# Optimization experiments

Measured on AMD Instinct MI355X. Metric: run time of the kernel, lower is better.

Reference implementation:

```python
import jax, jax.numpy as jnp
import numpy as np

B, T, E, H, V = 64, 32, 512, 512, 32000


def setup_inputs() -> dict:
    key = jax.random.key(0)
    ks = jax.random.split(key, 9)
    s = 0.05
    return {
        "features": jax.random.normal(ks[0], (B, E), jnp.float32),
        "captions": jax.random.randint(ks[1], (B, T), 0, V),
        "seq_len": T,
        "embed_table": jax.random.normal(ks[2], (V, E), jnp.float32) * s,
        "W_ih": jax.random.normal(ks[3], (4 * H, E), jnp.float32) * s,
        "W_hh": jax.random.normal(ks[4], (4 * H, H), jnp.float32) * s,
        "b_ih": jax.random.normal(ks[5], (4 * H,), jnp.float32) * s,
        "b_hh": jax.random.normal(ks[6], (4 * H,), jnp.float32) * s,
        "W_out": jax.random.normal(ks[7], (V, H), jnp.float32) * s,
        "b_out": jax.random.normal(ks[8], (V,), jnp.float32) * s,
    }


def _lstm_cell(x, h, c, W_ih, W_hh, b_ih, b_hh):
    # gates: (B, 4H), PyTorch LSTMCell gate order i, f, g, o
    gates = x @ W_ih.T + b_ih + h @ W_hh.T + b_hh
    i, f, g, o = jnp.split(gates, 4, axis=-1)
    c_new = jax.nn.sigmoid(f) * c + jax.nn.sigmoid(i) * jnp.tanh(g)
    h_new = jax.nn.sigmoid(o) * jnp.tanh(c_new)
    return h_new, c_new


def reference(features, captions, seq_len, embed_table, W_ih, W_hh, b_ih, b_hh, W_out, b_out):
    batch = features.shape[0]
    hdim = W_hh.shape[1]
    h0 = jnp.zeros((batch, hdim), features.dtype)
    c0 = jnp.zeros((batch, hdim), features.dtype)
    # prime the state with image features
    h, c = _lstm_cell(features, h0, c0, W_ih, W_hh, b_ih, b_hh)

    cap_emb = embed_table[captions]          # (B, T, E)
    xs = jnp.swapaxes(cap_emb, 0, 1)         # (T, B, E) for scan

    def step(carry, x_t):
        h, c = carry
        h, c = _lstm_cell(x_t, h, c, W_ih, W_hh, b_ih, b_hh)
        # dropout is identity in eval mode
        out = h @ W_out.T + b_out             # (B, V)
        return (h, c), out

    _, outs = jax.lax.scan(step, (h, c), xs)  # (T, B, V)
    return jnp.swapaxes(outs, 0, 1)           # (B, T, V)
```

## Files before the change

kernel.cpp:

```cpp
#include <hip/hip_runtime.h>
#include <stdint.h>

#define BB 64
#define TT 32
#define EE 512
#define HH 512
#define VV 32000
#define G4 2048

typedef _Float16 f16x8 __attribute__((ext_vector_type(8)));
typedef float f32x4 __attribute__((ext_vector_type(4)));

__device__ __forceinline__ unsigned short f2h(float f) {
  return __builtin_bit_cast(unsigned short, (_Float16)f);
}
__device__ __forceinline__ void gload_lds16(const unsigned short* g, unsigned short* l) {
  __builtin_amdgcn_global_load_lds((const __attribute__((address_space(1))) void*)g,
                                   (__attribute__((address_space(3))) void*)l, 16, 0, 0);
}
__device__ __forceinline__ float sigm(float x) { return 1.f / (1.f + __expf(-x)); }
__device__ __forceinline__ float tanh_fast(float x) {
  return 1.f - 2.f / (__expf(2.f * x) + 1.f);
}

__global__ __launch_bounds__(256) void k_gemm_ih(const float* __restrict__ feat,
                                                 const int* __restrict__ cap,
                                                 const float* __restrict__ emb,
                                                 const float* __restrict__ Bw,
                                                 const float* __restrict__ bih,
                                                 const float* __restrict__ bhh,
                                                 float* __restrict__ C) {
  __shared__ float As[16][128];
  __shared__ float Bs[16][128];
  const int tid = threadIdx.x;
  const int bx = blockIdx.x & 15;
  const int by = blockIdx.x >> 4;
  const int m0 = by * 128, n0 = bx * 128;
  const int tx = tid & 15, ty = tid >> 4;

  float acc[8][8];
#pragma unroll
  for (int i = 0; i < 8; i++)
#pragma unroll
    for (int j = 0; j < 8; j++) acc[i][j] = 0.f;

  const int lr = tid >> 1;
  const int lk = (tid & 1) * 8;
  int arow = m0 + lr; if (arow > 2111) arow = 2111;
  const float* Ap;
  if (arow < BB) {
    Ap = feat + (size_t)arow * EE + lk;
  } else {
    int idx = arow - BB;
    int t = idx >> 6, b = idx & 63;
    Ap = emb + (size_t)cap[b * TT + t] * EE + lk;
  }
  const int brow = n0 + lr;
  const float* Bp = Bw + (size_t)brow * EE + lk;

  for (int k0 = 0; k0 < EE; k0 += 16) {
    float4 a0 = *(const float4*)(Ap + k0);
    float4 a1 = *(const float4*)(Ap + k0 + 4);
    float4 b0 = *(const float4*)(Bp + k0);
    float4 b1 = *(const float4*)(Bp + k0 + 4);
    __syncthreads();
    As[lk + 0][lr] = a0.x; As[lk + 1][lr] = a0.y; As[lk + 2][lr] = a0.z; As[lk + 3][lr] = a0.w;
    As[lk + 4][lr] = a1.x; As[lk + 5][lr] = a1.y; As[lk + 6][lr] = a1.z; As[lk + 7][lr] = a1.w;
    Bs[lk + 0][lr] = b0.x; Bs[lk + 1][lr] = b0.y; Bs[lk + 2][lr] = b0.z; Bs[lk + 3][lr] = b0.w;
    Bs[lk + 4][lr] = b1.x; Bs[lk + 5][lr] = b1.y; Bs[lk + 6][lr] = b1.z; Bs[lk + 7][lr] = b1.w;
    __syncthreads();
#pragma unroll
    for (int k = 0; k < 16; k++) {
      float a[8], b[8];
      *(float4*)&a[0] = *(const float4*)&As[k][ty * 8];
      *(float4*)&a[4] = *(const float4*)&As[k][ty * 8 + 4];
      *(float4*)&b[0] = *(const float4*)&Bs[k][tx * 8];
      *(float4*)&b[4] = *(const float4*)&Bs[k][tx * 8 + 4];
#pragma unroll
      for (int i = 0; i < 8; i++)
#pragma unroll
        for (int j = 0; j < 8; j++) acc[i][j] += a[i] * b[j];
    }
  }

  float bs[8];
#pragma unroll
  for (int j = 0; j < 8; j++) {
    int n = n0 + tx * 8 + j;
    bs[j] = bih[n] + bhh[n];
  }
#pragma unroll
  for (int i = 0; i < 8; i++) {
    int m = m0 + ty * 8 + i;
    if (m < 2112) {
      float4 o0, o1;
      o0.x = acc[i][0] + bs[0]; o0.y = acc[i][1] + bs[1];
      o0.z = acc[i][2] + bs[2]; o0.w = acc[i][3] + bs[3];
      o1.x = acc[i][4] + bs[4]; o1.y = acc[i][5] + bs[5];
      o1.z = acc[i][6] + bs[6]; o1.w = acc[i][7] + bs[7];
      *(float4*)(C + (size_t)m * G4 + n0 + tx * 8) = o0;
      *(float4*)(C + (size_t)m * G4 + n0 + tx * 8 + 4) = o1;
    }
  }
}

__global__ void k_zero(int* ctr) {
  if (threadIdx.x < 33)
    __hip_atomic_store(&ctr[threadIdx.x], 0, __ATOMIC_RELAXED, __HIP_MEMORY_SCOPE_AGENT);
}

__global__ __launch_bounds__(512) void k_fused(const float* __restrict__ Gpre,
                                               const float* __restrict__ Whh,
                                               const float* __restrict__ Wout,
                                               const float* __restrict__ bout,
                                               char* hseq_base,
                                               float* __restrict__ out,
                                               int* __restrict__ ctr) {
  __shared__ __align__(16) char lds_raw[65536];
  unsigned short* hseq16 = (unsigned short*)hseq_base;
  unsigned int* hseq32 = (unsigned int*)hseq_base;

  const int tid = threadIdx.x;
  const int bid = blockIdx.x;
  const int l = tid & 63;
  const int w = tid >> 6;

  if (bid < 64) {
    unsigned short* W_lds = (unsigned short*)lds_raw;
    float* gate_buf = (float*)(lds_raw + 32768);
    const int u0 = bid * 8;
    const int lr = l & 15;
    const int kc = l >> 4;
    const int nt = w & 1;
    const int mt = w >> 1;
    const int es = w * 8 + (l >> 3);
    const int edu = l & 7;

    {
      int row = tid >> 4;
      int sub = tid & 15;
      int g = row >> 3, du = row & 7;
      const float* srcp = Whh + (size_t)(g * 512 + u0 + du) * HH;
#pragma unroll
      for (int c0 = 0; c0 < 4; ++c0) {
        int c = sub * 4 + c0;
        float4 va = *(const float4*)(srcp + c * 8);
        float4 vb = *(const float4*)(srcp + c * 8 + 4);
        __align__(16) unsigned short t8[8];
        t8[0] = f2h(va.x); t8[1] = f2h(va.y); t8[2] = f2h(va.z); t8[3] = f2h(va.w);
        t8[4] = f2h(vb.x); t8[5] = f2h(vb.y); t8[6] = f2h(vb.z); t8[7] = f2h(vb.w);
        *(int4*)((char*)W_lds + row * 1024 + ((c ^ (row & 7)) * 16)) = *(const int4*)t8;
      }
    }

    float c_reg;
    {
      const float* gp = Gpre + (size_t)es * G4 + u0 + edu;
      float gi = gp[0], gg = gp[1024], go = gp[1536];
      float cn = sigm(gi) * tanh_fast(gg);
      float hn = sigm(go) * tanh_fast(cn);
      c_reg = cn;
      unsigned int hb = f2h(hn);
      unsigned int other = (unsigned int)__shfl_xor((int)hb, 1);
      if (!(l & 1))
        __hip_atomic_store(&hseq32[(size_t)es * 256 + bid * 4 + (edu >> 1)],
                           hb | (other << 16), __ATOMIC_RELAXED, __HIP_MEMORY_SCOPE_AGENT);
    }
    asm volatile("s_waitcnt vmcnt(0)" ::: "memory");
    __syncthreads();
    if (tid == 0)
      __hip_atomic_fetch_add(&ctr[0], 1, __ATOMIC_RELAXED, __HIP_MEMORY_SCOPE_AGENT);

    float pre[4];
#pragma unroll
    for (int g = 0; g < 4; ++g)
      pre[g] = Gpre[((size_t)64 + es) * G4 + g * 512 + u0 + edu];

    if (tid == 0) {
      while (__hip_atomic_load(&ctr[0], __ATOMIC_RELAXED, __HIP_MEMORY_SCOPE_AGENT) < 64)
        __builtin_amdgcn_s_sleep(1);
    }
    __syncthreads();

    for (int s = 1; s <= TT; ++s) {
      const unsigned short* hin = hseq16 + (size_t)(s - 1) * BB * HH;
      f32x4 acca = {0.f, 0.f, 0.f, 0.f};
      f32x4 accb = {0.f, 0.f, 0.f, 0.f};
      const unsigned short* hbase = hin + (size_t)(mt * 16 + lr) * HH + kc * 8;
      const int wrow = nt * 16 + lr;
      const char* wbase = (const char*)W_lds + wrow * 1024;
#pragma unroll
      for (int kk = 0; kk < 8; ++kk) {
        uint4 hq0 = *(const uint4*)(hbase + kk * 32);
        int4 wq0 = *(const int4*)(wbase + (((kk * 4 + kc) ^ (wrow & 7)) * 16));
        acca = __builtin_amdgcn_mfma_f32_16x16x32_f16(
            __builtin_bit_cast(f16x8, hq0), __builtin_bit_cast(f16x8, wq0), acca, 0, 0, 0);
        uint4 hq1 = *(const uint4*)(hbase + (kk + 8) * 32);
        int4 wq1 = *(const int4*)(wbase + ((((kk + 8) * 4 + kc) ^ (wrow & 7)) * 16));
        accb = __builtin_amdgcn_mfma_f32_16x16x32_f16(
            __builtin_bit_cast(f16x8, hq1), __builtin_bit_cast(f16x8, wq1), accb, 0, 0, 0);
      }
      f32x4 acc;
#pragma unroll
      for (int j = 0; j < 4; ++j) acc[j] = acca[j] + accb[j];

      {
        int g = nt * 2 + (lr >> 3);
        int du = lr & 7;
#pragma unroll
        for (int j = 0; j < 4; ++j) {
          int ss = mt * 16 + kc * 4 + j;
          gate_buf[g * 512 + du * 64 + (ss ^ (du << 3))] = acc[j];
        }
      }
      __syncthreads();

      {
        float gi = gate_buf[0 * 512 + edu * 64 + (es ^ (edu << 3))] + pre[0];
        float gf = gate_buf[1 * 512 + edu * 64 + (es ^ (edu << 3))] + pre[1];
        float gg = gate_buf[2 * 512 + edu * 64 + (es ^ (edu << 3))] + pre[2];
        float go = gate_buf[3 * 512 + edu * 64 + (es ^ (edu << 3))] + pre[3];
        float cn = sigm(gf) * c_reg + sigm(gi) * tanh_fast(gg);
        float hn = sigm(go) * tanh_fast(cn);
        c_reg = cn;
        unsigned int hb = f2h(hn);
        unsigned int other = (unsigned int)__shfl_xor((int)hb, 1);
        if (!(l & 1))
          __hip_atomic_store(&hseq32[(size_t)s * 16384 + es * 256 + bid * 4 + (edu >> 1)],
                             hb | (other << 16), __ATOMIC_RELAXED, __HIP_MEMORY_SCOPE_AGENT);
      }
      asm volatile("s_waitcnt vmcnt(0)" ::: "memory");
      __syncthreads();
      if (tid == 0)
        __hip_atomic_fetch_add(&ctr[s], 1, __ATOMIC_RELAXED, __HIP_MEMORY_SCOPE_AGENT);

      if (s < TT) {
#pragma unroll
        for (int g = 0; g < 4; ++g)
          pre[g] = Gpre[((size_t)(s + 1) * 64 + es) * G4 + g * 512 + u0 + edu];
        if (tid == 0) {
          while (__hip_atomic_load(&ctr[s], __ATOMIC_RELAXED, __HIP_MEMORY_SCOPE_AGENT) < 64)
            __builtin_amdgcn_s_sleep(1);
        }
        __syncthreads();
      }
    }
  } else {
    unsigned short* As = (unsigned short*)lds_raw;
    const int slice0 = bid - 64;
    const bool two = (slice0 < 58);
    const int n00 = slice0 * 128;
    const int n01 = (two ? (slice0 + 192) : slice0) * 128;
    const int bcol = w * 16 + (l >> 4) * 4;
    const float4 bo0 = *(const float4*)(bout + n00 + bcol);
    const float4 bo1 = *(const float4*)(bout + n01 + bcol);

    const int vr0 = n00 + w * 16 + (l & 15);
    const int vr1 = n01 + w * 16 + (l & 15);
    const int kb = (l >> 4) * 8;
    uint4 w0r[16], w1r[16];
#pragma unroll
    for (int kt = 0; kt < 16; ++kt) {
      const float* p = Wout + (size_t)vr0 * HH + kt * 32 + kb;
      float4 a = *(const float4*)p;
      float4 b = *(const float4*)(p + 4);
      __align__(16) unsigned short t8[8];
      t8[0] = f2h(a.x); t8[1] = f2h(a.y); t8[2] = f2h(a.z); t8[3] = f2h(a.w);
      t8[4] = f2h(b.x); t8[5] = f2h(b.y); t8[6] = f2h(b.z); t8[7] = f2h(b.w);
      w0r[kt] = *(const uint4*)t8;
    }
    if (two) {
#pragma unroll
      for (int kt = 0; kt < 16; ++kt) {
        const float* p = Wout + (size_t)vr1 * HH + kt * 32 + kb;
        float4 a = *(const float4*)p;
        float4 b = *(const float4*)(p + 4);
        __align__(16) unsigned short t8[8];
        t8[0] = f2h(a.x); t8[1] = f2h(a.y); t8[2] = f2h(a.z); t8[3] = f2h(a.w);
        t8[4] = f2h(b.x); t8[5] = f2h(b.y); t8[6] = f2h(b.z); t8[7] = f2h(b.w);
        w1r[kt] = *(const uint4*)t8;
      }
    }

    for (int s = 1; s <= TT; ++s) {
      if (tid == 0) {
        while (__hip_atomic_load(&ctr[s], __ATOMIC_RELAXED, __HIP_MEMORY_SCOPE_AGENT) < 64)
          __builtin_amdgcn_s_sleep(4);
      }
      __syncthreads();

      const unsigned short* hs = hseq16 + (size_t)s * BB * HH;
#pragma unroll
      for (int it = 0; it < 8; ++it) {
        int ci = it * 512 + tid;
        int row = ci >> 6, cd = ci & 63;
        gload_lds16(hs + (size_t)row * 512 + (cd ^ (row & 7)) * 8, As + ci * 8);
      }
      asm volatile("s_waitcnt vmcnt(0)" ::: "memory");
      __syncthreads();

      f32x4 acc0[4], acc1[4];
#pragma unroll
      for (int m = 0; m < 4; ++m) {
        acc0[m] = (f32x4){0.f, 0.f, 0.f, 0.f};
        acc1[m] = (f32x4){0.f, 0.f, 0.f, 0.f};
      }
#pragma unroll
      for (int m = 0; m < 4; ++m) {
        int row = m * 16 + (l & 15);
#pragma unroll
        for (int kt = 0; kt < 16; ++kt) {
          int c = kt * 4 + (l >> 4);
          f16x8 af = *(const f16x8*)&As[row * 512 + (c ^ (row & 7)) * 8];
          acc0[m] = __builtin_amdgcn_mfma_f32_16x16x32_f16(
              __builtin_bit_cast(f16x8, w0r[kt]), af, acc0[m], 0, 0, 0);
          if (two)
            acc1[m] = __builtin_amdgcn_mfma_f32_16x16x32_f16(
                __builtin_bit_cast(f16x8, w1r[kt]), af, acc1[m], 0, 0, 0);
        }
      }

#pragma unroll
      for (int m = 0; m < 4; ++m) {
        int b = m * 16 + (l & 15);
        float* orow0 = out + ((size_t)(b * TT + (s - 1))) * VV + n00 + bcol;
        float4 v;
        v.x = acc0[m][0] + bo0.x;
        v.y = acc0[m][1] + bo0.y;
        v.z = acc0[m][2] + bo0.z;
        v.w = acc0[m][3] + bo0.w;
        *(float4*)orow0 = v;
        if (two) {
          float* orow1 = out + ((size_t)(b * TT + (s - 1))) * VV + n01 + bcol;
          float4 v1;
          v1.x = acc1[m][0] + bo1.x;
          v1.y = acc1[m][1] + bo1.y;
          v1.z = acc1[m][2] + bo1.z;
          v1.w = acc1[m][3] + bo1.w;
          *(float4*)orow1 = v1;
        }
      }
    }
  }
}

extern "C" void kernel_launch(void* const* d_in, const int* in_sizes, int n_in,
                              void* d_out, int out_size, void* d_ws, size_t ws_size,
                              hipStream_t stream) {
  const float* feat = (const float*)d_in[0];
  const int* cap = (const int*)d_in[1];
  const float* emb = (const float*)d_in[3];
  const float* Wih = (const float*)d_in[4];
  const float* Whh = (const float*)d_in[5];
  const float* bih = (const float*)d_in[6];
  const float* bhh = (const float*)d_in[7];
  const float* Wout = (const float*)d_in[8];
  const float* bout = (const float*)d_in[9];
  float* out = (float*)d_out;

  char* ws = (char*)d_ws;
  float* Gpre = (float*)ws;
  char* hseq = ws + 17301504;
  int* ctr = (int*)(ws + 19464192);

  k_zero<<<dim3(1), dim3(64), 0, stream>>>(ctr);
  k_gemm_ih<<<dim3(17 * 16), dim3(256), 0, stream>>>(feat, cap, emb, Wih, bih, bhh, Gpre);
  k_fused<<<dim3(256), dim3(512), 0, stream>>>(Gpre, Whh, Wout, bout, hseq, out, ctr);
}
```

Before: 454.1 us.

## Replace atomic counter barrier with per-block flags and aggregator broadcast

Replaces the shared per-step atomic counter that all 256 blocks spin on with per-block progress flags, each on its own 128-byte line. Block 0 gathers all 64 recurrent blocks' flags with one wavefront and then publishes the step number to 16 replicated 'done' lines, which the other blocks poll. The goal is to cut atomic contention and polling traffic on a single cache line during the 32 serial step barriers. In exchange, every barrier adds an extra hop through the aggregator block, which sits on the critical path of the recurrence.

```diff
diff --git a/kernel.cpp b/kernel.cpp
--- a/kernel.cpp
+++ b/kernel.cpp
@@ -104,9 +104,35 @@
   }
 }
 
-__global__ void k_zero(int* ctr) {
-  if (threadIdx.x < 33)
-    __hip_atomic_store(&ctr[threadIdx.x], 0, __ATOMIC_RELAXED, __HIP_MEMORY_SCOPE_AGENT);
+__global__ void k_zero(int* f) {
+  for (int i = threadIdx.x; i < 2560; i += 256)
+    __hip_atomic_store(&f[i], 0, __ATOMIC_RELAXED, __HIP_MEMORY_SCOPE_AGENT);
+}
+
+__device__ __forceinline__ void agg_phase(int* arr, int* done, int tid, int p) {
+  if (tid < 64) {
+    for (;;) {
+      int v = __hip_atomic_load(&arr[tid * 32], __ATOMIC_RELAXED, __HIP_MEMORY_SCOPE_AGENT);
+      if (__all(v >= p)) break;
+      __builtin_amdgcn_s_sleep(1);
+    }
+    if (tid == 0) {
+#pragma unroll
+      for (int c = 0; c < 16; ++c)
+        __hip_atomic_store(&done[c * 32], p, __ATOMIC_RELAXED, __HIP_MEMORY_SCOPE_AGENT);
+    }
+  }
+}
+
+__device__ __forceinline__ void tree_wait(int* arr, int* done, int bid, int tid, int p) {
+  if (bid == 0) {
+    agg_phase(arr, done, tid, p);
+  } else if (tid == 0) {
+    while (__hip_atomic_load(&done[(bid & 15) * 32], __ATOMIC_RELAXED,
+                             __HIP_MEMORY_SCOPE_AGENT) < p)
+      __builtin_amdgcn_s_sleep(1);
+  }
+  __syncthreads();
 }
 
 __global__ __launch_bounds__(512) void k_fused(const float* __restrict__ Gpre,
@@ -115,10 +141,12 @@
                                                const float* __restrict__ bout,
                                                char* hseq_base,
                                                float* __restrict__ out,
-                                               int* __restrict__ ctr) {
+                                               int* __restrict__ flags) {
   __shared__ __align__(16) char lds_raw[65536];
   unsigned short* hseq16 = (unsigned short*)hseq_base;
   unsigned int* hseq32 = (unsigned int*)hseq_base;
+  int* arr = flags;
+  int* done = flags + 2048;
 
   const int tid = threadIdx.x;
   const int bid = blockIdx.x;
@@ -169,18 +197,14 @@
     asm volatile("s_waitcnt vmcnt(0)" ::: "memory");
     __syncthreads();
     if (tid == 0)
-      __hip_atomic_fetch_add(&ctr[0], 1, __ATOMIC_RELAXED, __HIP_MEMORY_SCOPE_AGENT);
+      __hip_atomic_store(&arr[bid * 32], 1, __ATOMIC_RELAXED, __HIP_MEMORY_SCOPE_AGENT);
 
     float pre[4];
 #pragma unroll
     for (int g = 0; g < 4; ++g)
       pre[g] = Gpre[((size_t)64 + es) * G4 + g * 512 + u0 + edu];
 
-    if (tid == 0) {
-      while (__hip_atomic_load(&ctr[0], __ATOMIC_RELAXED, __HIP_MEMORY_SCOPE_AGENT) < 64)
-        __builtin_amdgcn_s_sleep(1);
-    }
-    __syncthreads();
+    tree_wait(arr, done, bid, tid, 1);
 
     for (int s = 1; s <= TT; ++s) {
       const unsigned short* hin = hseq16 + (size_t)(s - 1) * BB * HH;
@@ -232,19 +256,17 @@
       asm volatile("s_waitcnt vmcnt(0)" ::: "memory");
       __syncthreads();
       if (tid == 0)
-        __hip_atomic_fetch_add(&ctr[s], 1, __ATOMIC_RELAXED, __HIP_MEMORY_SCOPE_AGENT);
+        __hip_atomic_store(&arr[bid * 32], s + 1, __ATOMIC_RELAXED, __HIP_MEMORY_SCOPE_AGENT);
 
       if (s < TT) {
 #pragma unroll
         for (int g = 0; g < 4; ++g)
           pre[g] = Gpre[((size_t)(s + 1) * 64 + es) * G4 + g * 512 + u0 + edu];
-        if (tid == 0) {
-          while (__hip_atomic_load(&ctr[s], __ATOMIC_RELAXED, __HIP_MEMORY_SCOPE_AGENT) < 64)
-            __builtin_amdgcn_s_sleep(1);
-        }
-        __syncthreads();
-      }
-    }
+        tree_wait(arr, done, bid, tid, s + 1);
+      }
+    }
+
+    if (bid == 0) agg_phase(arr, done, tid, TT + 1);
   } else {
     unsigned short* As = (unsigned short*)lds_raw;
     const int slice0 = bid - 64;
@@ -284,8 +306,9 @@
 
     for (int s = 1; s <= TT; ++s) {
       if (tid == 0) {
-        while (__hip_atomic_load(&ctr[s], __ATOMIC_RELAXED, __HIP_MEMORY_SCOPE_AGENT) < 64)
-          __builtin_amdgcn_s_sleep(4);
+        while (__hip_atomic_load(&done[(bid & 15) * 32], __ATOMIC_RELAXED,
+                                 __HIP_MEMORY_SCOPE_AGENT) < s + 1)
+          __builtin_amdgcn_s_sleep(2);
       }
       __syncthreads();
 
@@ -361,9 +384,9 @@
   char* ws = (char*)d_ws;
   float* Gpre = (float*)ws;
   char* hseq = ws + 17301504;
-  int* ctr = (int*)(ws + 19464192);
-
-  k_zero<<<dim3(1), dim3(64), 0, stream>>>(ctr);
+  int* flags = (int*)(ws + 19464192);
+
+  k_zero<<<dim3(1), dim3(256), 0, stream>>>(flags);
   k_gemm_ih<<<dim3(17 * 16), dim3(256), 0, stream>>>(feat, cap, emb, Wih, bih, bhh, Gpre);
-  k_fused<<<dim3(256), dim3(512), 0, stream>>>(Gpre, Whh, Wout, bout, hseq, out, ctr);
-}
+  k_fused<<<dim3(256), dim3(512), 0, stream>>>(Gpre, Whh, Wout, bout, hseq, out, flags);
+}
```

New measurement: 448.1 us. No clear change (-1.3%).

## Split fused RNN/output kernel into separate recurrence and output-projection kernels

Applied to the files above, without the earlier changes.

Replaces the single persistent kernel, where 64 blocks ran the LSTM recurrence and 192 blocks streamed the vocab projection step by step, with two kernels. The recurrence kernel uses a per-block flag grid barrier instead of per-step counters. A separate 250-block output GEMM then runs after all hidden states exist. This removes the cross-block polling and the two-slice imbalance in the projection, but gives up overlapping the projection with the serial recurrence. It also drops the split accumulator in the recurrent MFMA loop and replaces the zeroing kernel with a memset.

```diff
diff --git a/kernel.cpp b/kernel.cpp
--- a/kernel.cpp
+++ b/kernel.cpp
@@ -104,242 +104,190 @@
   }
 }
 
-__global__ void k_zero(int* ctr) {
-  if (threadIdx.x < 33)
-    __hip_atomic_store(&ctr[threadIdx.x], 0, __ATOMIC_RELAXED, __HIP_MEMORY_SCOPE_AGENT);
-}
-
-__global__ __launch_bounds__(512) void k_fused(const float* __restrict__ Gpre,
-                                               const float* __restrict__ Whh,
-                                               const float* __restrict__ Wout,
-                                               const float* __restrict__ bout,
-                                               char* hseq_base,
-                                               float* __restrict__ out,
-                                               int* __restrict__ ctr) {
-  __shared__ __align__(16) char lds_raw[65536];
+__device__ __forceinline__ void gridbar_nf(int* flags, int id) {
+  asm volatile("s_waitcnt vmcnt(0)" ::: "memory");
+  __syncthreads();
+  if (threadIdx.x == 0)
+    __hip_atomic_store(&flags[blockIdx.x], id, __ATOMIC_RELAXED, __HIP_MEMORY_SCOPE_AGENT);
+  if (threadIdx.x < 64) {
+    while (__hip_atomic_load(&flags[threadIdx.x], __ATOMIC_RELAXED, __HIP_MEMORY_SCOPE_AGENT) < id)
+      __builtin_amdgcn_s_sleep(1);
+  }
+  __syncthreads();
+}
+
+__global__ __launch_bounds__(512) void k_rnn(const float* __restrict__ Gpre,
+                                             const float* __restrict__ Whh,
+                                             char* hseq_base,
+                                             int* __restrict__ flags) {
+  __shared__ __align__(16) unsigned short W_lds[32 * 512];
+  __shared__ float gate_buf[2048];
   unsigned short* hseq16 = (unsigned short*)hseq_base;
   unsigned int* hseq32 = (unsigned int*)hseq_base;
 
   const int tid = threadIdx.x;
   const int bid = blockIdx.x;
+  const int u0 = bid * 8;
   const int l = tid & 63;
   const int w = tid >> 6;
-
-  if (bid < 64) {
-    unsigned short* W_lds = (unsigned short*)lds_raw;
-    float* gate_buf = (float*)(lds_raw + 32768);
-    const int u0 = bid * 8;
-    const int lr = l & 15;
-    const int kc = l >> 4;
-    const int nt = w & 1;
-    const int mt = w >> 1;
-    const int es = w * 8 + (l >> 3);
-    const int edu = l & 7;
+  const int lr = l & 15;
+  const int kc = l >> 4;
+  const int nt = w & 1;
+  const int mt = w >> 1;
+  const int es = w * 8 + (l >> 3);
+  const int edu = l & 7;
+
+  {
+    int row = tid >> 4;
+    int sub = tid & 15;
+    int g = row >> 3, du = row & 7;
+    const float* srcp = Whh + (size_t)(g * 512 + u0 + du) * HH;
+#pragma unroll
+    for (int c0 = 0; c0 < 4; ++c0) {
+      int c = sub * 4 + c0;
+      float4 va = *(const float4*)(srcp + c * 8);
+      float4 vb = *(const float4*)(srcp + c * 8 + 4);
+      __align__(16) unsigned short t8[8];
+      t8[0] = f2h(va.x); t8[1] = f2h(va.y); t8[2] = f2h(va.z); t8[3] = f2h(va.w);
+      t8[4] = f2h(vb.x); t8[5] = f2h(vb.y); t8[6] = f2h(vb.z); t8[7] = f2h(vb.w);
+      *(int4*)((char*)W_lds + row * 1024 + ((c ^ (row & 7)) * 16)) = *(const int4*)t8;
+    }
+  }
+
+  float c_reg;
+  {
+    const float* gp = Gpre + (size_t)es * G4 + u0 + edu;
+    float gi = gp[0], gg = gp[1024], go = gp[1536];
+    float cn = sigm(gi) * tanh_fast(gg);
+    float hn = sigm(go) * tanh_fast(cn);
+    c_reg = cn;
+    unsigned int hb = f2h(hn);
+    unsigned int other = (unsigned int)__shfl_xor((int)hb, 1);
+    if (!(l & 1))
+      __hip_atomic_store(&hseq32[(size_t)es * 256 + bid * 4 + (edu >> 1)],
+                         hb | (other << 16), __ATOMIC_RELAXED, __HIP_MEMORY_SCOPE_AGENT);
+  }
+
+  float pre[4];
+#pragma unroll
+  for (int g = 0; g < 4; ++g)
+    pre[g] = Gpre[((size_t)(1 * 64) + es) * G4 + g * 512 + u0 + edu];
+
+  gridbar_nf(flags, 1);
+
+  for (int s = 1; s <= TT; ++s) {
+    const unsigned short* hin = hseq16 + (size_t)(s - 1) * BB * HH;
+
+    f32x4 acc = {0.f, 0.f, 0.f, 0.f};
+    const unsigned short* hbase = hin + (size_t)(mt * 16 + lr) * HH + kc * 8;
+    const int wrow = nt * 16 + lr;
+    const char* wbase = (const char*)W_lds + wrow * 1024;
+#pragma unroll
+    for (int kk = 0; kk < 16; ++kk) {
+      uint4 hq = *(const uint4*)(hbase + kk * 32);
+      int4 wq = *(const int4*)(wbase + (((kk * 4 + kc) ^ (wrow & 7)) * 16));
+      f16x8 hf = __builtin_bit_cast(f16x8, hq);
+      f16x8 wf = __builtin_bit_cast(f16x8, wq);
+      acc = __builtin_amdgcn_mfma_f32_16x16x32_f16(hf, wf, acc, 0, 0, 0);
+    }
 
     {
-      int row = tid >> 4;
-      int sub = tid & 15;
-      int g = row >> 3, du = row & 7;
-      const float* srcp = Whh + (size_t)(g * 512 + u0 + du) * HH;
-#pragma unroll
-      for (int c0 = 0; c0 < 4; ++c0) {
-        int c = sub * 4 + c0;
-        float4 va = *(const float4*)(srcp + c * 8);
-        float4 vb = *(const float4*)(srcp + c * 8 + 4);
-        __align__(16) unsigned short t8[8];
-        t8[0] = f2h(va.x); t8[1] = f2h(va.y); t8[2] = f2h(va.z); t8[3] = f2h(va.w);
-        t8[4] = f2h(vb.x); t8[5] = f2h(vb.y); t8[6] = f2h(vb.z); t8[7] = f2h(vb.w);
-        *(int4*)((char*)W_lds + row * 1024 + ((c ^ (row & 7)) * 16)) = *(const int4*)t8;
+      int g = nt * 2 + (lr >> 3);
+      int du = lr & 7;
+#pragma unroll
+      for (int j = 0; j < 4; ++j) {
+        int ss = mt * 16 + kc * 4 + j;
+        gate_buf[g * 512 + du * 64 + (ss ^ (du << 3))] = acc[j];
       }
     }
-
-    float c_reg;
+    __syncthreads();
+
     {
-      const float* gp = Gpre + (size_t)es * G4 + u0 + edu;
-      float gi = gp[0], gg = gp[1024], go = gp[1536];
-      float cn = sigm(gi) * tanh_fast(gg);
+      float gi = gate_buf[0 * 512 + edu * 64 + (es ^ (edu << 3))] + pre[0];
+      float gf = gate_buf[1 * 512 + edu * 64 + (es ^ (edu << 3))] + pre[1];
+      float gg = gate_buf[2 * 512 + edu * 64 + (es ^ (edu << 3))] + pre[2];
+      float go = gate_buf[3 * 512 + edu * 64 + (es ^ (edu << 3))] + pre[3];
+      float cn = sigm(gf) * c_reg + sigm(gi) * tanh_fast(gg);
       float hn = sigm(go) * tanh_fast(cn);
       c_reg = cn;
       unsigned int hb = f2h(hn);
       unsigned int other = (unsigned int)__shfl_xor((int)hb, 1);
       if (!(l & 1))
-        __hip_atomic_store(&hseq32[(size_t)es * 256 + bid * 4 + (edu >> 1)],
+        __hip_atomic_store(&hseq32[(size_t)s * 16384 + es * 256 + bid * 4 + (edu >> 1)],
                            hb | (other << 16), __ATOMIC_RELAXED, __HIP_MEMORY_SCOPE_AGENT);
+    }
+
+    if (s < TT) {
+#pragma unroll
+      for (int g = 0; g < 4; ++g)
+        pre[g] = Gpre[((size_t)(s + 1) * 64 + es) * G4 + g * 512 + u0 + edu];
+      gridbar_nf(flags, s + 1);
+    }
+  }
+}
+
+__global__ __launch_bounds__(512) void k_gemm_out(const unsigned short* __restrict__ hseq,
+                                                  const float* __restrict__ Wout,
+                                                  const float* __restrict__ bout,
+                                                  float* __restrict__ out) {
+  __shared__ __align__(16) unsigned short As[BB * HH];
+  const int tid = threadIdx.x;
+  const int l = tid & 63;
+  const int w = tid >> 6;
+  const int n00 = blockIdx.x * 128;
+  const int bcol = w * 16 + (l >> 4) * 4;
+  const float4 bo0 = *(const float4*)(bout + n00 + bcol);
+
+  const int vr0 = n00 + w * 16 + (l & 15);
+  const int kb = (l >> 4) * 8;
+  uint4 w0r[16];
+#pragma unroll
+  for (int kt = 0; kt < 16; ++kt) {
+    const float* p = Wout + (size_t)vr0 * HH + kt * 32 + kb;
+    float4 a = *(const float4*)p;
+    float4 b = *(const float4*)(p + 4);
+    __align__(16) unsigned short t8[8];
+    t8[0] = f2h(a.x); t8[1] = f2h(a.y); t8[2] = f2h(a.z); t8[3] = f2h(a.w);
+    t8[4] = f2h(b.x); t8[5] = f2h(b.y); t8[6] = f2h(b.z); t8[7] = f2h(b.w);
+    w0r[kt] = *(const uint4*)t8;
+  }
+
+  for (int s = 1; s <= TT; ++s) {
+    if (s > 1) __syncthreads();
+    const unsigned short* hs = hseq + (size_t)s * (BB * HH);
+#pragma unroll
+    for (int it = 0; it < 8; ++it) {
+      int ci = it * 512 + tid;
+      int row = ci >> 6, cd = ci & 63;
+      gload_lds16(hs + (size_t)row * HH + (cd ^ (row & 7)) * 8, As + ci * 8);
     }
     asm volatile("s_waitcnt vmcnt(0)" ::: "memory");
     __syncthreads();
-    if (tid == 0)
-      __hip_atomic_fetch_add(&ctr[0], 1, __ATOMIC_RELAXED, __HIP_MEMORY_SCOPE_AGENT);
-
-    float pre[4];
-#pragma unroll
-    for (int g = 0; g < 4; ++g)
-      pre[g] = Gpre[((size_t)64 + es) * G4 + g * 512 + u0 + edu];
-
-    if (tid == 0) {
-      while (__hip_atomic_load(&ctr[0], __ATOMIC_RELAXED, __HIP_MEMORY_SCOPE_AGENT) < 64)
-        __builtin_amdgcn_s_sleep(1);
-    }
-    __syncthreads();
-
-    for (int s = 1; s <= TT; ++s) {
-      const unsigned short* hin = hseq16 + (size_t)(s - 1) * BB * HH;
-      f32x4 acca = {0.f, 0.f, 0.f, 0.f};
-      f32x4 accb = {0.f, 0.f, 0.f, 0.f};
-      const unsigned short* hbase = hin + (size_t)(mt * 16 + lr) * HH + kc * 8;
-      const int wrow = nt * 16 + lr;
-      const char* wbase = (const char*)W_lds + wrow * 1024;
-#pragma unroll
-      for (int kk = 0; kk < 8; ++kk) {
-        uint4 hq0 = *(const uint4*)(hbase + kk * 32);
-        int4 wq0 = *(const int4*)(wbase + (((kk * 4 + kc) ^ (wrow & 7)) * 16));
-        acca = __builtin_amdgcn_mfma_f32_16x16x32_f16(
-            __builtin_bit_cast(f16x8, hq0), __builtin_bit_cast(f16x8, wq0), acca, 0, 0, 0);
-        uint4 hq1 = *(const uint4*)(hbase + (kk + 8) * 32);
-        int4 wq1 = *(const int4*)(wbase + ((((kk + 8) * 4 + kc) ^ (wrow & 7)) * 16));
-        accb = __builtin_amdgcn_mfma_f32_16x16x32_f16(
-            __builtin_bit_cast(f16x8, hq1), __builtin_bit_cast(f16x8, wq1), accb, 0, 0, 0);
+
+    f32x4 acc0[4];
+#pragma unroll
+    for (int m = 0; m < 4; ++m) acc0[m] = (f32x4){0.f, 0.f, 0.f, 0.f};
+#pragma unroll
+    for (int m = 0; m < 4; ++m) {
+      int row = m * 16 + (l & 15);
+#pragma unroll
+      for (int kt = 0; kt < 16; ++kt) {
+        int c = kt * 4 + (l >> 4);
+        f16x8 af = *(const f16x8*)&As[row * HH + (c ^ (row & 7)) * 8];
+        acc0[m] = __builtin_amdgcn_mfma_f32_16x16x32_f16(
+            __builtin_bit_cast(f16x8, w0r[kt]), af, acc0[m], 0, 0, 0);
       }
-      f32x4 acc;
-#pragma unroll
-      for (int j = 0; j < 4; ++j) acc[j] = acca[j] + accb[j];
-
-      {
-        int g = nt * 2 + (lr >> 3);
-        int du = lr & 7;
-#pragma unroll
-        for (int j = 0; j < 4; ++j) {
-          int ss = mt * 16 + kc * 4 + j;
-          gate_buf[g * 512 + du * 64 + (ss ^ (du << 3))] = acc[j];
-        }
-      }
-      __syncthreads();
-
-      {
-        float gi = gate_buf[0 * 512 + edu * 64 + (es ^ (edu << 3))] + pre[0];
-        float gf = gate_buf[1 * 512 + edu * 64 + (es ^ (edu << 3))] + pre[1];
-        float gg = gate_buf[2 * 512 + edu * 64 + (es ^ (edu << 3))] + pre[2];
-        float go = gate_buf[3 * 512 + edu * 64 + (es ^ (edu << 3))] + pre[3];
-        float cn = sigm(gf) * c_reg + sigm(gi) * tanh_fast(gg);
-        float hn = sigm(go) * tanh_fast(cn);
-        c_reg = cn;
-        unsigned int hb = f2h(hn);
-        unsigned int other = (unsigned int)__shfl_xor((int)hb, 1);
-        if (!(l & 1))
-          __hip_atomic_store(&hseq32[(size_t)s * 16384 + es * 256 + bid * 4 + (edu >> 1)],
-                             hb | (other << 16), __ATOMIC_RELAXED, __HIP_MEMORY_SCOPE_AGENT);
-      }
-      asm volatile("s_waitcnt vmcnt(0)" ::: "memory");
-      __syncthreads();
-      if (tid == 0)
-        __hip_atomic_fetch_add(&ctr[s], 1, __ATOMIC_RELAXED, __HIP_MEMORY_SCOPE_AGENT);
-
-      if (s < TT) {
-#pragma unroll
-        for (int g = 0; g < 4; ++g)
-          pre[g] = Gpre[((size_t)(s + 1) * 64 + es) * G4 + g * 512 + u0 + edu];
-        if (tid == 0) {
-          while (__hip_atomic_load(&ctr[s], __ATOMIC_RELAXED, __HIP_MEMORY_SCOPE_AGENT) < 64)
-            __builtin_amdgcn_s_sleep(1);
-        }
-        __syncthreads();
-      }
-    }
-  } else {
-    unsigned short* As = (unsigned short*)lds_raw;
-    const int slice0 = bid - 64;
-    const bool two = (slice0 < 58);
-    const int n00 = slice0 * 128;
-    const int n01 = (two ? (slice0 + 192) : slice0) * 128;
-    const int bcol = w * 16 + (l >> 4) * 4;
-    const float4 bo0 = *(const float4*)(bout + n00 + bcol);
-    const float4 bo1 = *(const float4*)(bout + n01 + bcol);
-
-    const int vr0 = n00 + w * 16 + (l & 15);
-    const int vr1 = n01 + w * 16 + (l & 15);
-    const int kb = (l >> 4) * 8;
-    uint4 w0r[16], w1r[16];
-#pragma unroll
-    for (int kt = 0; kt < 16; ++kt) {
-      const float* p = Wout + (size_t)vr0 * HH + kt * 32 + kb;
-      float4 a = *(const float4*)p;
-      float4 b = *(const float4*)(p + 4);
-      __align__(16) unsigned short t8[8];
-      t8[0] = f2h(a.x); t8[1] = f2h(a.y); t8[2] = f2h(a.z); t8[3] = f2h(a.w);
-      t8[4] = f2h(b.x); t8[5] = f2h(b.y); t8[6] = f2h(b.z); t8[7] = f2h(b.w);
-      w0r[kt] = *(const uint4*)t8;
-    }
-    if (two) {
-#pragma unroll
-      for (int kt = 0; kt < 16; ++kt) {
-        const float* p = Wout + (size_t)vr1 * HH + kt * 32 + kb;
-        float4 a = *(const float4*)p;
-        float4 b = *(const float4*)(p + 4);
-        __align__(16) unsigned short t8[8];
-        t8[0] = f2h(a.x); t8[1] = f2h(a.y); t8[2] = f2h(a.z); t8[3] = f2h(a.w);
-        t8[4] = f2h(b.x); t8[5] = f2h(b.y); t8[6] = f2h(b.z); t8[7] = f2h(b.w);
-        w1r[kt] = *(const uint4*)t8;
-      }
-    }
-
-    for (int s = 1; s <= TT; ++s) {
-      if (tid == 0) {
-        while (__hip_atomic_load(&ctr[s], __ATOMIC_RELAXED, __HIP_MEMORY_SCOPE_AGENT) < 64)
-          __builtin_amdgcn_s_sleep(4);
-      }
-      __syncthreads();
-
-      const unsigned short* hs = hseq16 + (size_t)s * BB * HH;
-#pragma unroll
-      for (int it = 0; it < 8; ++it) {
-        int ci = it * 512 + tid;
-        int row = ci >> 6, cd = ci & 63;
-        gload_lds16(hs + (size_t)row * 512 + (cd ^ (row & 7)) * 8, As + ci * 8);
-      }
-      asm volatile("s_waitcnt vmcnt(0)" ::: "memory");
-      __syncthreads();
-
-      f32x4 acc0[4], acc1[4];
-#pragma unroll
-      for (int m = 0; m < 4; ++m) {
-        acc0[m] = (f32x4){0.f, 0.f, 0.f, 0.f};
-        acc1[m] = (f32x4){0.f, 0.f, 0.f, 0.f};
-      }
-#pragma unroll
-      for (int m = 0; m < 4; ++m) {
-        int row = m * 16 + (l & 15);
-#pragma unroll
-        for (int kt = 0; kt < 16; ++kt) {
-          int c = kt * 4 + (l >> 4);
-          f16x8 af = *(const f16x8*)&As[row * 512 + (c ^ (row & 7)) * 8];
-          acc0[m] = __builtin_amdgcn_mfma_f32_16x16x32_f16(
-              __builtin_bit_cast(f16x8, w0r[kt]), af, acc0[m], 0, 0, 0);
-          if (two)
-            acc1[m] = __builtin_amdgcn_mfma_f32_16x16x32_f16(
-                __builtin_bit_cast(f16x8, w1r[kt]), af, acc1[m], 0, 0, 0);
-        }
-      }
-
-#pragma unroll
-      for (int m = 0; m < 4; ++m) {
-        int b = m * 16 + (l & 15);
-        float* orow0 = out + ((size_t)(b * TT + (s - 1))) * VV + n00 + bcol;
-        float4 v;
-        v.x = acc0[m][0] + bo0.x;
-        v.y = acc0[m][1] + bo0.y;
-        v.z = acc0[m][2] + bo0.z;
-        v.w = acc0[m][3] + bo0.w;
-        *(float4*)orow0 = v;
-        if (two) {
-          float* orow1 = out + ((size_t)(b * TT + (s - 1))) * VV + n01 + bcol;
-          float4 v1;
-          v1.x = acc1[m][0] + bo1.x;
-          v1.y = acc1[m][1] + bo1.y;
-          v1.z = acc1[m][2] + bo1.z;
-          v1.w = acc1[m][3] + bo1.w;
-          *(float4*)orow1 = v1;
-        }
-      }
+    }
+#pragma unroll
+    for (int m = 0; m < 4; ++m) {
+      int b = m * 16 + (l & 15);
+      float* orow = out + ((size_t)(b * TT + (s - 1))) * VV + n00 + bcol;
+      float4 v;
+      v.x = acc0[m][0] + bo0.x;
+      v.y = acc0[m][1] + bo0.y;
+      v.z = acc0[m][2] + bo0.z;
+      v.w = acc0[m][3] + bo0.w;
+      *(float4*)orow = v;
     }
   }
 }
@@ -361,9 +309,10 @@
   char* ws = (char*)d_ws;
   float* Gpre = (float*)ws;
   char* hseq = ws + 17301504;
-  int* ctr = (int*)(ws + 19464192);
-
-  k_zero<<<dim3(1), dim3(64), 0, stream>>>(ctr);
+  int* flags = (int*)(ws + 19464192);
+
+  hipMemsetAsync(flags, 0, 4096, stream);
   k_gemm_ih<<<dim3(17 * 16), dim3(256), 0, stream>>>(feat, cap, emb, Wih, bih, bhh, Gpre);
-  k_fused<<<dim3(256), dim3(512), 0, stream>>>(Gpre, Whh, Wout, bout, hseq, out, ctr);
-}
+  k_rnn<<<dim3(64), dim3(512), 0, stream>>>(Gpre, Whh, hseq, flags);
+  k_gemm_out<<<dim3(250), dim3(512), 0, stream>>>((const unsigned short*)hseq, Wout, bout, out);
+}
```

Result: slower. 479.8 us (+5.7%).
